# Kernel optimization log

Hardware: AMD Instinct MI355X
Metric: run time of the kernel (lower is better)

Reference implementation:

```python
import jax, jax.numpy as jnp
import numpy as np

B, IN, H = 8192, 1024, 1024

def _ln(x, g, b, eps=1e-5):
    mu = jnp.mean(x, axis=-1, keepdims=True)
    var = jnp.mean(jnp.square(x - mu), axis=-1, keepdims=True)
    return (x - mu) * jax.lax.rsqrt(var + eps) * g + b

def setup_inputs() -> dict:
    key = jax.random.key(0)
    ks = jax.random.split(key, 8)
    s_h = 1.0 / np.sqrt(H)
    s_i = 1.0 / np.sqrt(IN)
    inp = {
        'x': jax.random.normal(ks[0], (B, IN), jnp.float32),
        'h': jax.random.normal(ks[1], (B, H), jnp.float32),
        'W_r': jax.random.uniform(ks[2], (H, H), jnp.float32, -s_h, s_h),
        'U_r': jax.random.uniform(ks[3], (H, IN), jnp.float32, -s_i, s_i),
        'W_u': jax.random.uniform(ks[4], (H, H), jnp.float32, -s_h, s_h),
        'U_u': jax.random.uniform(ks[5], (H, IN), jnp.float32, -s_i, s_i),
        'W_c': jax.random.uniform(ks[6], (H, H), jnp.float32, -s_h, s_h),
        'U_c': jax.random.uniform(ks[7], (H, IN), jnp.float32, -s_i, s_i),
        # LayerNorm params: rows = [r_hidden, r_input, u_hidden, u_input, c_hidden, c_input]
        'ln_gamma': 0.1 * jnp.ones((6, H), jnp.float32),
        'ln_beta': jnp.zeros((6, H), jnp.float32),
    }
    return inp

def reference(x, h, W_r, U_r, W_u, U_u, W_c, U_c, ln_gamma, ln_beta):
    g, b = ln_gamma, ln_beta
    # nn.Linear(bias=False): y = x @ W.T
    r = jax.nn.sigmoid(_ln(h @ W_r.T, g[0], b[0]) + _ln(x @ U_r.T, g[1], b[1]))
    u = jax.nn.sigmoid(_ln(h @ W_u.T, g[2], b[2]) + _ln(x @ U_u.T, g[3], b[3]))
    c = jnp.tanh(_ln((h * r) @ W_c.T, g[4], b[4]) + _ln(x @ U_c.T, g[5], b[5]))
    return (1.0 - u) * h + u * c
```

## Files before the change

kernel.cpp:

```cpp
#include <hip/hip_runtime.h>
#include <cstdint>
#include <cstddef>

typedef unsigned short u16;
typedef unsigned char u8;
typedef __attribute__((ext_vector_type(8))) short bf16x8;
typedef __attribute__((ext_vector_type(4))) float f32x4;
typedef __attribute__((ext_vector_type(4))) int i32x4;
typedef __attribute__((ext_vector_type(8))) int i32x8;

__device__ inline float bf2f(u16 u) { return __uint_as_float(((unsigned)u) << 16); }
__device__ inline unsigned f2bf(float f) {
  unsigned u = __float_as_uint(f);
  u += 0x7fffu + ((u >> 16) & 1u);
  return u >> 16;
}

__device__ inline unsigned f2fp8(float f) {
  unsigned s = (__float_as_uint(f) >> 31) << 7;
  float a = fabsf(f);
  if (a >= 0.015625f) {
    unsigned u = __float_as_uint(a);
    u += 0x7FFFFu + ((u >> 20) & 1u);
    unsigned e = (u >> 23) - 120u;
    unsigned m = (u >> 20) & 7u;
    return s | (e << 3) | m;
  }
  int m = (int)rintf(a * 512.0f);
  return s | (unsigned)m;
}

__device__ inline void async16(const void* g, void* l) {
  __builtin_amdgcn_global_load_lds(
      (const __attribute__((address_space(1))) void*)g,
      (__attribute__((address_space(3))) void*)l, 16, 0, 0);
}

__device__ inline i32x8 join8(i32x4 lo, i32x4 hi) {
  i32x8 r;
  r[0] = lo[0]; r[1] = lo[1]; r[2] = lo[2]; r[3] = lo[3];
  r[4] = hi[0]; r[5] = hi[1]; r[6] = hi[2]; r[7] = hi[3];
  return r;
}

__device__ inline void unpack8(uint4 q, float* o) {
  o[0] = bf2f((u16)(q.x & 0xffffu)); o[1] = bf2f((u16)(q.x >> 16));
  o[2] = bf2f((u16)(q.y & 0xffffu)); o[3] = bf2f((u16)(q.y >> 16));
  o[4] = bf2f((u16)(q.z & 0xffffu)); o[5] = bf2f((u16)(q.z >> 16));
  o[6] = bf2f((u16)(q.w & 0xffffu)); o[7] = bf2f((u16)(q.w >> 16));
}

__device__ inline uint4 pack8(const float* v) {
  uint4 q;
  q.x = f2bf(v[0]) | (f2bf(v[1]) << 16);
  q.y = f2bf(v[2]) | (f2bf(v[3]) << 16);
  q.z = f2bf(v[4]) | (f2bf(v[5]) << 16);
  q.w = f2bf(v[6]) | (f2bf(v[7]) << 16);
  return q;
}

__device__ inline float fast_sigmoid(float z) {
  return 1.0f / (1.0f + exp2f(-1.4426950408889634f * z));
}
__device__ inline float fast_tanh(float z) {
  return 1.0f - 2.0f / (1.0f + exp2f(2.8853900817779268f * z));
}

struct ConvArgs2 {
  const float* x; const float* h; const float* wr; const float* ur;
  const float* wbf[4];
  u16* xb; u16* hb; u8* x8; u8* h8; u8* w8r; u8* w8u;
  u16* wbo[4];
};

__global__ __launch_bounds__(256) void convert_all(ConvArgs2 a) {
  const int b = blockIdx.x;
  const int t = threadIdx.x;
  if (b < 16384) {
    const bool isx = b < 8192;
    const int off = isx ? b : b - 8192;
    const float* __restrict__ s = isx ? a.x : a.h;
    u16* __restrict__ db = isx ? a.xb : a.hb;
    u8*  __restrict__ d8 = isx ? a.x8 : a.h8;
    const int i = (off * 256 + t) * 4;
    float4 v = *(const float4*)(s + i);
    uint2 o;
    o.x = f2bf(v.x) | (f2bf(v.y) << 16);
    o.y = f2bf(v.z) | (f2bf(v.w) << 16);
    *(uint2*)(db + i) = o;
    unsigned q = f2fp8(v.x) | (f2fp8(v.y) << 8) | (f2fp8(v.z) << 16) | (f2fp8(v.w) << 24);
    *(unsigned*)(d8 + i) = q;
  } else if (b < 18432) {
    const bool isr = b < 17408;
    const int off = isr ? b - 16384 : b - 17408;
    const float* __restrict__ s = isr ? a.wr : a.ur;
    u8* __restrict__ d8 = isr ? a.w8r : a.w8u;
    const int i = (off * 256 + t) * 4;
    float4 v = *(const float4*)(s + i);
    unsigned q = f2fp8(v.x * 8192.f) | (f2fp8(v.y * 8192.f) << 8) |
                 (f2fp8(v.z * 8192.f) << 16) | (f2fp8(v.w * 8192.f) << 24);
    *(unsigned*)(d8 + i) = q;
  } else {
    const int tt = b - 18432;
    const int which = tt >> 10;
    const int off = tt & 1023;
    const float* __restrict__ s = a.wbf[which];
    u16* __restrict__ d = a.wbo[which];
    const int i = (off * 256 + t) * 4;
    float4 v = *(const float4*)(s + i);
    uint2 o;
    o.x = f2bf(v.x) | (f2bf(v.y) << 16);
    o.y = f2bf(v.z) | (f2bf(v.w) << 16);
    *(uint2*)(d + i) = o;
  }
}

struct GemmF8 { const u8* A[2]; const u8* Bw[2]; u16* Y[2]; };

__global__ __launch_bounds__(256) void gemm_fp8(GemmF8 args) {
  const int p = blockIdx.x;
  const int xcd = p & 7;
  const int s = p >> 3;
  const int pr = s >> 4;
  const int cc = s & 15;
  const int gate = cc >> 3;
  const int col = cc & 7;
  const int r = pr * 8 + xcd;

  const u8* __restrict__ A  = args.A[gate];
  const u8* __restrict__ Bw = args.Bw[gate];
  u16* __restrict__ Y = args.Y[gate];

  __shared__ __attribute__((aligned(16))) u8 As[128 * 128];
  __shared__ __attribute__((aligned(16))) u8 Bs[128 * 128];

  const int tid  = threadIdx.x;
  const int lane = tid & 63;
  const int w    = tid >> 6;
  const int wm   = w >> 1;
  const int wn   = w & 1;

  const int rowBlk = r * 128;
  const int colBlk = col * 128;

  const int srow = lane >> 3;
  const int scol = ((lane & 7) ^ srow) * 16;
  const u8* gA[4]; const u8* gB[4]; u8* lA[4]; u8* lB[4];
#pragma unroll
  for (int i = 0; i < 4; i++) {
    const int rr = w * 32 + i * 8;
    gA[i] = A  + (size_t)(rowBlk + rr + srow) * 1024 + scol;
    gB[i] = Bw + (size_t)(colBlk + rr + srow) * 1024 + scol;
    lA[i] = &As[rr * 128];
    lB[i] = &Bs[rr * 128];
  }

  const int sw = lane & 7;
  const int g0 = (lane >> 4) * 2;
  const int o0 = ((g0 ^ sw) << 4);
  const int o1 = (((g0 + 1) ^ sw) << 4);
  const int frA = (wm * 64 + (lane & 15)) * 128;
  const int frB = (wn * 64 + (lane & 15)) * 128;

  f32x4 acc[4][4] = {};

  for (int k0 = 0; k0 < 1024; k0 += 128) {
#pragma unroll
    for (int i = 0; i < 4; i++) {
      async16(gA[i] + k0, lA[i]);
      async16(gB[i] + k0, lB[i]);
    }
    __syncthreads();
    i32x8 af[4], bfr[4];
#pragma unroll
    for (int t = 0; t < 4; t++) {
      const int ra = frA + t * 16 * 128;
      const int rb = frB + t * 16 * 128;
      af[t]  = join8(*(const i32x4*)&As[ra + o0], *(const i32x4*)&As[ra + o1]);
      bfr[t] = join8(*(const i32x4*)&Bs[rb + o0], *(const i32x4*)&Bs[rb + o1]);
    }
#pragma unroll
    for (int tm = 0; tm < 4; tm++)
#pragma unroll
      for (int tn = 0; tn < 4; tn++)
        acc[tm][tn] = __builtin_amdgcn_mfma_scale_f32_16x16x128_f8f6f4(
            af[tm], bfr[tn], acc[tm][tn],
            0, 0,
            0, 127,
            0, 114);
    __syncthreads();
  }

  const int rBase = rowBlk + wm * 64 + (lane >> 4) * 4;
  const int cBase = colBlk + wn * 64 + (lane & 15);
#pragma unroll
  for (int tm = 0; tm < 4; tm++) {
#pragma unroll
    for (int i = 0; i < 4; i++) {
      const size_t rr = (size_t)(rBase + tm * 16 + i);
#pragma unroll
      for (int tn = 0; tn < 4; tn++)
        Y[rr * 1024 + cBase + tn * 16] = (u16)f2bf(acc[tm][tn][i]);
    }
  }
}

struct Gemm4 { const u16* A[4]; const u16* Bw[4]; u16* Y[4]; };

__global__ __launch_bounds__(512, 2) void gemm_8ph(Gemm4 args) {
  const int p = blockIdx.x;
  const int wg = (p & 7) * 64 + (p >> 3);
  const int gate = wg >> 7;
  const int rem  = wg & 127;
  const int rblk = rem >> 2;
  const int cblk = rem & 3;

  const u16* __restrict__ A  = args.A[gate];
  const u16* __restrict__ Bw = args.Bw[gate];
  u16* __restrict__ Y = args.Y[gate];

  __shared__ __attribute__((aligned(16))) u16 sm[2][2][2][128 * 64];

  const int tid  = threadIdx.x;
  const int lane = tid & 63;
  const int w    = tid >> 6;
  const int wm   = w >> 2;
  const int wn   = w & 3;

  const int l8   = lane >> 3;
  const int sgrp = (lane & 7) ^ l8;
  const u16* aSrc = A  + ((size_t)(rblk * 256 + w * 8 + l8) << 10) + sgrp * 8;
  const u16* bSrc = Bw + ((size_t)(cblk * 256 + w * 8 + l8) << 10) + sgrp * 8;
  const int ldsW = w * 8 * 64;

  const int fr = (lane & 15) * 64 + ((((lane >> 4) ^ (lane & 7))) << 3);

  f32x4 acc_lo[4][4] = {};
  f32x4 acc_hi[4][4] = {};

  auto stage = [&](const u16* src, int tt, int op, int half) {
    const int d = tt & 1;
    const u16* s = src + (size_t)half * 131072 + tt * 64;
    u16* l0 = &sm[d][op][half][ldsW];
    async16(s, l0);
    async16(s + 65536, l0 + 4096);
  };

  stage(bSrc, 0, 1, 0); stage(bSrc, 0, 1, 1);
  stage(aSrc, 0, 0, 0); stage(aSrc, 0, 0, 1);
  stage(bSrc, 1, 1, 0); stage(bSrc, 1, 1, 1);
  stage(aSrc, 1, 0, 0);
  asm volatile("s_waitcnt vmcnt(6)" ::: "memory");
  __builtin_amdgcn_s_barrier();

  for (int t = 0; t < 16; ++t) {
    const int d = t & 1;
    const u16* baseA = &sm[d][0][wm][0];
    const u16* baseB = &sm[d][1][wn >> 1][(wn & 1) * 4096];

    bf16x8 alo[2][4], bfg[2][4];
#pragma unroll
    for (int kk = 0; kk < 2; ++kk) {
      const int fo = fr ^ (kk << 5);
#pragma unroll
      for (int m = 0; m < 4; ++m) alo[kk][m] = *(const bf16x8*)(baseA + m * 1024 + fo);
#pragma unroll
      for (int n = 0; n < 4; ++n) bfg[kk][n] = *(const bf16x8*)(baseB + n * 1024 + fo);
    }
    if (t + 1 < 16) stage(aSrc, t + 1, 0, 1);
    __builtin_amdgcn_s_barrier();
    asm volatile("s_waitcnt lgkmcnt(0)" ::: "memory");
    __builtin_amdgcn_s_setprio(1);
#pragma unroll
    for (int m = 0; m < 4; ++m)
#pragma unroll
      for (int n = 0; n < 2; ++n)
#pragma unroll
        for (int kk = 0; kk < 2; ++kk)
          acc_lo[m][n] = __builtin_amdgcn_mfma_f32_16x16x32_bf16(alo[kk][m], bfg[kk][n], acc_lo[m][n], 0, 0, 0);
    __builtin_amdgcn_s_setprio(0);
    __builtin_amdgcn_s_barrier();

    if (t + 2 < 16) stage(bSrc, t + 2, 1, 0);
    __builtin_amdgcn_s_barrier();
    __builtin_amdgcn_s_setprio(1);
#pragma unroll
    for (int m = 0; m < 4; ++m)
#pragma unroll
      for (int n = 2; n < 4; ++n)
#pragma unroll
        for (int kk = 0; kk < 2; ++kk)
          acc_lo[m][n] = __builtin_amdgcn_mfma_f32_16x16x32_bf16(alo[kk][m], bfg[kk][n], acc_lo[m][n], 0, 0, 0);
    __builtin_amdgcn_s_setprio(0);
    __builtin_amdgcn_s_barrier();

    bf16x8 ahi[2][4];
#pragma unroll
    for (int kk = 0; kk < 2; ++kk) {
      const int fo = fr ^ (kk << 5);
#pragma unroll
      for (int m = 0; m < 4; ++m) ahi[kk][m] = *(const bf16x8*)(baseA + (m + 4) * 1024 + fo);
    }
    if (t + 2 < 16) stage(bSrc, t + 2, 1, 1);
    __builtin_amdgcn_s_barrier();
    asm volatile("s_waitcnt lgkmcnt(0)" ::: "memory");
    __builtin_amdgcn_s_setprio(1);
#pragma unroll
    for (int m = 0; m < 4; ++m)
#pragma unroll
      for (int n = 0; n < 2; ++n)
#pragma unroll
        for (int kk = 0; kk < 2; ++kk)
          acc_hi[m][n] = __builtin_amdgcn_mfma_f32_16x16x32_bf16(ahi[kk][m], bfg[kk][n], acc_hi[m][n], 0, 0, 0);
    __builtin_amdgcn_s_setprio(0);
    __builtin_amdgcn_s_barrier();

    if (t + 2 < 16) stage(aSrc, t + 2, 0, 0);
    __builtin_amdgcn_s_barrier();
    __builtin_amdgcn_s_setprio(1);
#pragma unroll
    for (int m = 0; m < 4; ++m)
#pragma unroll
      for (int n = 2; n < 4; ++n)
#pragma unroll
        for (int kk = 0; kk < 2; ++kk)
          acc_hi[m][n] = __builtin_amdgcn_mfma_f32_16x16x32_bf16(ahi[kk][m], bfg[kk][n], acc_hi[m][n], 0, 0, 0);
    __builtin_amdgcn_s_setprio(0);
    if (t < 14) asm volatile("s_waitcnt vmcnt(6)" ::: "memory");
    else        asm volatile("s_waitcnt vmcnt(0)" ::: "memory");
    __builtin_amdgcn_s_barrier();
  }

  const int rBase = rblk * 256 + wm * 128 + (lane >> 4) * 4;
  const int cBase = cblk * 256 + wn * 64 + (lane & 15);
#pragma unroll
  for (int m = 0; m < 4; ++m) {
#pragma unroll
    for (int i = 0; i < 4; ++i) {
      const size_t r0 = (size_t)(rBase + m * 16 + i) * 1024 + cBase;
#pragma unroll
      for (int n = 0; n < 4; ++n) {
        Y[r0 + n * 16]             = (u16)f2bf(acc_lo[m][n][i]);
        Y[r0 + 64 * 1024 + n * 16] = (u16)f2bf(acc_hi[m][n][i]);
      }
    }
  }
}

__global__ __launch_bounds__(256) void rgate_kernel(
    const u16* __restrict__ Yrh, const u16* __restrict__ Yrx,
    const u16* __restrict__ hb, const float* __restrict__ gamma,
    const float* __restrict__ beta, u16* __restrict__ hrb) {
  const int row  = blockIdx.x * 4 + (threadIdx.x >> 6);
  const int lane = threadIdx.x & 63;
  const size_t rb = (size_t)row * 1024;

  uint4 qa[2], qb[2], qh[2];
  qa[0] = *(const uint4*)(Yrh + rb + lane * 8);
  qa[1] = *(const uint4*)(Yrh + rb + 512 + lane * 8);
  qb[0] = *(const uint4*)(Yrx + rb + lane * 8);
  qb[1] = *(const uint4*)(Yrx + rb + 512 + lane * 8);
  qh[0] = *(const uint4*)(hb  + rb + lane * 8);
  qh[1] = *(const uint4*)(hb  + rb + 512 + lane * 8);

  float s0 = 0.f, s0q = 0.f, s1 = 0.f, s1q = 0.f;
  float tmp[8];
#pragma unroll
  for (int c = 0; c < 2; c++) {
    unpack8(qa[c], tmp);
#pragma unroll
    for (int j = 0; j < 8; j++) { s0 += tmp[j]; s0q += tmp[j] * tmp[j]; }
    unpack8(qb[c], tmp);
#pragma unroll
    for (int j = 0; j < 8; j++) { s1 += tmp[j]; s1q += tmp[j] * tmp[j]; }
  }
#pragma unroll
  for (int off = 1; off < 64; off <<= 1) {
    s0 += __shfl_xor(s0, off, 64);  s0q += __shfl_xor(s0q, off, 64);
    s1 += __shfl_xor(s1, off, 64);  s1q += __shfl_xor(s1q, off, 64);
  }

  const float inv = 1.0f / 1024.0f;
  const float mu0 = s0 * inv, rs0 = rsqrtf(s0q * inv - mu0 * mu0 + 1e-5f);
  const float mu1 = s1 * inv, rs1 = rsqrtf(s1q * inv - mu1 * mu1 + 1e-5f);

#pragma unroll
  for (int c = 0; c < 2; c++) {
    const int cb = c * 512 + lane * 8;
    float va[8], vb[8], vh[8], o[8];
    unpack8(qa[c], va); unpack8(qb[c], vb); unpack8(qh[c], vh);
#pragma unroll
    for (int j = 0; j < 8; j++) {
      const float ln0 = (va[j] - mu0) * rs0 * gamma[cb + j] + beta[cb + j];
      const float ln1 = (vb[j] - mu1) * rs1 * gamma[1024 + cb + j] + beta[1024 + cb + j];
      const float rg = fast_sigmoid(ln0 + ln1);
      o[j] = vh[j] * rg;
    }
    *(uint4*)(hrb + rb + cb) = pack8(o);
  }
}

__global__ __launch_bounds__(256) void final_fuse(
    const u16* __restrict__ Yuh, const u16* __restrict__ Yux,
    const u16* __restrict__ Ych, const u16* __restrict__ Ycx,
    const float* __restrict__ h, const float* __restrict__ gamma,
    const float* __restrict__ beta, float* __restrict__ out) {
  const int row  = blockIdx.x * 4 + (threadIdx.x >> 6);
  const int lane = threadIdx.x & 63;
  const size_t rb = (size_t)row * 1024;

  uint4 q0[2], q1[2], q2[2], q3[2];
  float4 hf[4];
#pragma unroll
  for (int c = 0; c < 2; c++) {
    const int cb = c * 512 + lane * 8;
    q0[c] = *(const uint4*)(Yuh + rb + cb);
    q1[c] = *(const uint4*)(Yux + rb + cb);
    q2[c] = *(const uint4*)(Ych + rb + cb);
    q3[c] = *(const uint4*)(Ycx + rb + cb);
    hf[c * 2]     = *(const float4*)(h + rb + cb);
    hf[c * 2 + 1] = *(const float4*)(h + rb + cb + 4);
  }

  float s[8] = {0.f, 0.f, 0.f, 0.f, 0.f, 0.f, 0.f, 0.f};
  float tmp[8];
#pragma unroll
  for (int c = 0; c < 2; c++) {
    unpack8(q0[c], tmp);
#pragma unroll
    for (int j = 0; j < 8; j++) { s[0] += tmp[j]; s[1] += tmp[j] * tmp[j]; }
    unpack8(q1[c], tmp);
#pragma unroll
    for (int j = 0; j < 8; j++) { s[2] += tmp[j]; s[3] += tmp[j] * tmp[j]; }
    unpack8(q2[c], tmp);
#pragma unroll
    for (int j = 0; j < 8; j++) { s[4] += tmp[j]; s[5] += tmp[j] * tmp[j]; }
    unpack8(q3[c], tmp);
#pragma unroll
    for (int j = 0; j < 8; j++) { s[6] += tmp[j]; s[7] += tmp[j] * tmp[j]; }
  }
#pragma unroll
  for (int off = 1; off < 64; off <<= 1) {
#pragma unroll
    for (int q = 0; q < 8; q++) s[q] += __shfl_xor(s[q], off, 64);
  }

  const float inv = 1.0f / 1024.0f;
  const float mu0 = s[0] * inv, rs0 = rsqrtf(s[1] * inv - mu0 * mu0 + 1e-5f);
  const float mu1 = s[2] * inv, rs1 = rsqrtf(s[3] * inv - mu1 * mu1 + 1e-5f);
  const float mu2 = s[4] * inv, rs2 = rsqrtf(s[5] * inv - mu2 * mu2 + 1e-5f);
  const float mu3 = s[6] * inv, rs3 = rsqrtf(s[7] * inv - mu3 * mu3 + 1e-5f);

#pragma unroll
  for (int c = 0; c < 2; c++) {
    const int cb = c * 512 + lane * 8;
    float v0[8], v1[8], v2[8], v3[8];
    unpack8(q0[c], v0); unpack8(q1[c], v1); unpack8(q2[c], v2); unpack8(q3[c], v3);
    const float* hv = (const float*)&hf[c * 2];
    float o[8];
#pragma unroll
    for (int j = 0; j < 8; j++) {
      const int cc = cb + j;
      const float ln2 = (v0[j] - mu0) * rs0 * gamma[2 * 1024 + cc] + beta[2 * 1024 + cc];
      const float ln3 = (v1[j] - mu1) * rs1 * gamma[3 * 1024 + cc] + beta[3 * 1024 + cc];
      const float ln4 = (v2[j] - mu2) * rs2 * gamma[4 * 1024 + cc] + beta[4 * 1024 + cc];
      const float ln5 = (v3[j] - mu3) * rs3 * gamma[5 * 1024 + cc] + beta[5 * 1024 + cc];
      const float u  = fast_sigmoid(ln2 + ln3);
      const float cg = fast_tanh(ln4 + ln5);
      o[j] = (1.0f - u) * hv[j] + u * cg;
    }
    *(float4*)(out + rb + cb)     = *(float4*)&o[0];
    *(float4*)(out + rb + cb + 4) = *(float4*)&o[4];
  }
}

extern "C" void kernel_launch(void* const* d_in, const int* in_sizes, int n_in,
                              void* d_out, int out_size, void* d_ws, size_t ws_size,
                              hipStream_t stream) {
  const float* x  = (const float*)d_in[0];
  const float* h  = (const float*)d_in[1];
  const float* W_r = (const float*)d_in[2];
  const float* U_r = (const float*)d_in[3];
  const float* W_u = (const float*)d_in[4];
  const float* U_u = (const float*)d_in[5];
  const float* W_c = (const float*)d_in[6];
  const float* U_c = (const float*)d_in[7];
  const float* gamma = (const float*)d_in[8];
  const float* beta  = (const float*)d_in[9];
  float* out = (float*)d_out;

  char* ws = (char*)d_ws;
  const size_t MB = 1024 * 1024;
  const size_t SZ_ACT = 16 * MB;

  u16* xb = (u16*)(ws);
  u16* hb = (u16*)(ws + 16 * MB);
  u16* wb[4];
  for (int i = 0; i < 4; i++) wb[i] = (u16*)(ws + (32 + 2 * i) * MB);
  u8* w8r = (u8*)(ws + 40 * MB);
  u8* w8u = (u8*)(ws + 41 * MB);
  char* ybase = ws + 42 * MB;
  u16* Y0 = (u16*)(ybase);
  u16* Y1 = (u16*)(ybase + SZ_ACT);
  u16* Y2 = (u16*)(ybase + 2 * SZ_ACT);
  u16* Y3 = (u16*)(ybase + 3 * SZ_ACT);
  u16* Y5 = (u16*)(ybase + 4 * SZ_ACT);
  u8* x8 = (u8*)Y5;
  u8* h8 = (u8*)Y5 + 8 * MB;

  ConvArgs2 ca = {};
  ca.x = x; ca.h = h; ca.wr = W_r; ca.ur = U_r;
  ca.wbf[0] = W_u; ca.wbf[1] = U_u; ca.wbf[2] = W_c; ca.wbf[3] = U_c;
  ca.xb = xb; ca.hb = hb; ca.x8 = x8; ca.h8 = h8; ca.w8r = w8r; ca.w8u = w8u;
  ca.wbo[0] = (u16*)(ws + 32 * MB); ca.wbo[1] = (u16*)(ws + 34 * MB);
  ca.wbo[2] = (u16*)(ws + 36 * MB); ca.wbo[3] = (u16*)(ws + 38 * MB);
  convert_all<<<22528, 256, 0, stream>>>(ca);

  GemmF8 gf = {};
  gf.A[0] = h8; gf.Bw[0] = w8r; gf.Y[0] = Y0;
  gf.A[1] = x8; gf.Bw[1] = w8u; gf.Y[1] = Y1;
  gemm_fp8<<<1024, 256, 0, stream>>>(gf);

  rgate_kernel<<<2048, 256, 0, stream>>>(Y0, Y1, hb, gamma, beta, Y1);

  Gemm4 gb = {};
  gb.A[0] = xb; gb.Bw[0] = wb[1]; gb.Y[0] = Y3;
  gb.A[1] = xb; gb.Bw[1] = wb[3]; gb.Y[1] = Y5;
  gb.A[2] = hb; gb.Bw[2] = wb[0]; gb.Y[2] = Y2;
  gb.A[3] = Y1; gb.Bw[3] = wb[2]; gb.Y[3] = Y0;
  gemm_8ph<<<512, 512, 0, stream>>>(gb);

  final_fuse<<<2048, 256, 0, stream>>>(Y2, Y3, Y0, Y5, h, gamma, beta, out);
}
```

Before: 270.9 us.

## Rewrite FP8 GEMM as 256x256 tiles with double-buffered phased pipeline

Replaces the 128x128, 4-wave FP8 GEMM with a 256x256, 8-wave kernel that double-buffers LDS tiles and interleaves async global->LDS loads with MFMA phases, guarded by explicit barriers, waitcnts and setprio. Larger tiles raise data reuse per block, and the phased schedule is meant to hide load latency that the old load-sync-compute loop exposed. In exchange there are fewer blocks (256 for 256 CUs), higher register and LDS use (128KB LDS per block), and the hand-written vmcnt counts have to stay correct.

After: 270.4 us. About the same (-0.2%).

```diff
diff --git a/kernel.cpp b/kernel.cpp
--- a/kernel.cpp
+++ b/kernel.cpp
@@ -117,90 +117,143 @@
 
 struct GemmF8 { const u8* A[2]; const u8* Bw[2]; u16* Y[2]; };
 
-__global__ __launch_bounds__(256) void gemm_fp8(GemmF8 args) {
+__global__ __launch_bounds__(512, 2) void gemm_fp8(GemmF8 args) {
   const int p = blockIdx.x;
-  const int xcd = p & 7;
-  const int s = p >> 3;
-  const int pr = s >> 4;
-  const int cc = s & 15;
-  const int gate = cc >> 3;
-  const int col = cc & 7;
-  const int r = pr * 8 + xcd;
+  const int wg = (p & 7) * 32 + (p >> 3);
+  const int gate = wg >> 7;
+  const int rem  = wg & 127;
+  const int rblk = rem >> 2;
+  const int cblk = rem & 3;
 
   const u8* __restrict__ A  = args.A[gate];
   const u8* __restrict__ Bw = args.Bw[gate];
   u16* __restrict__ Y = args.Y[gate];
 
-  __shared__ __attribute__((aligned(16))) u8 As[128 * 128];
-  __shared__ __attribute__((aligned(16))) u8 Bs[128 * 128];
+  __shared__ __attribute__((aligned(16))) u8 sm[2][2][2][128 * 128];
 
   const int tid  = threadIdx.x;
   const int lane = tid & 63;
   const int w    = tid >> 6;
-  const int wm   = w >> 1;
-  const int wn   = w & 1;
-
-  const int rowBlk = r * 128;
-  const int colBlk = col * 128;
-
-  const int srow = lane >> 3;
-  const int scol = ((lane & 7) ^ srow) * 16;
-  const u8* gA[4]; const u8* gB[4]; u8* lA[4]; u8* lB[4];
-#pragma unroll
-  for (int i = 0; i < 4; i++) {
-    const int rr = w * 32 + i * 8;
-    gA[i] = A  + (size_t)(rowBlk + rr + srow) * 1024 + scol;
-    gB[i] = Bw + (size_t)(colBlk + rr + srow) * 1024 + scol;
-    lA[i] = &As[rr * 128];
-    lB[i] = &Bs[rr * 128];
-  }
+  const int wm   = w >> 2;
+  const int wn   = w & 3;
+
+  const int l8   = lane >> 3;
+  const int sgrp = (lane & 7) ^ l8;
+  const u8* aSrc = A  + ((size_t)(rblk * 256 + w * 8 + l8) << 10) + sgrp * 16;
+  const u8* bSrc = Bw + ((size_t)(cblk * 256 + w * 8 + l8) << 10) + sgrp * 16;
+  const int ldsW = w * 8 * 128;
 
   const int sw = lane & 7;
   const int g0 = (lane >> 4) * 2;
   const int o0 = ((g0 ^ sw) << 4);
   const int o1 = (((g0 + 1) ^ sw) << 4);
-  const int frA = (wm * 64 + (lane & 15)) * 128;
-  const int frB = (wn * 64 + (lane & 15)) * 128;
-
-  f32x4 acc[4][4] = {};
-
-  for (int k0 = 0; k0 < 1024; k0 += 128) {
-#pragma unroll
-    for (int i = 0; i < 4; i++) {
-      async16(gA[i] + k0, lA[i]);
-      async16(gB[i] + k0, lB[i]);
-    }
-    __syncthreads();
-    i32x8 af[4], bfr[4];
-#pragma unroll
-    for (int t = 0; t < 4; t++) {
-      const int ra = frA + t * 16 * 128;
-      const int rb = frB + t * 16 * 128;
-      af[t]  = join8(*(const i32x4*)&As[ra + o0], *(const i32x4*)&As[ra + o1]);
-      bfr[t] = join8(*(const i32x4*)&Bs[rb + o0], *(const i32x4*)&Bs[rb + o1]);
-    }
-#pragma unroll
-    for (int tm = 0; tm < 4; tm++)
-#pragma unroll
-      for (int tn = 0; tn < 4; tn++)
-        acc[tm][tn] = __builtin_amdgcn_mfma_scale_f32_16x16x128_f8f6f4(
-            af[tm], bfr[tn], acc[tm][tn],
-            0, 0,
-            0, 127,
-            0, 114);
-    __syncthreads();
-  }
-
-  const int rBase = rowBlk + wm * 64 + (lane >> 4) * 4;
-  const int cBase = colBlk + wn * 64 + (lane & 15);
-#pragma unroll
-  for (int tm = 0; tm < 4; tm++) {
-#pragma unroll
-    for (int i = 0; i < 4; i++) {
-      const size_t rr = (size_t)(rBase + tm * 16 + i);
-#pragma unroll
-      for (int tn = 0; tn < 4; tn++)
-        Y[rr * 1024 + cBase + tn * 16] = (u16)f2bf(acc[tm][tn][i]);
+  const int frR = (lane & 15) * 128;
+
+  f32x4 acc_lo[4][4] = {};
+  f32x4 acc_hi[4][4] = {};
+
+  auto stage = [&](const u8* src, int tt, int op, int half) {
+    const int d = tt & 1;
+    const u8* s = src + (size_t)half * 131072 + tt * 128;
+    u8* l0 = &sm[d][op][half][ldsW];
+    async16(s, l0);
+    async16(s + 65536, l0 + 8192);
+  };
+
+  stage(bSrc, 0, 1, 0); stage(bSrc, 0, 1, 1);
+  stage(aSrc, 0, 0, 0); stage(aSrc, 0, 0, 1);
+  stage(bSrc, 1, 1, 0); stage(bSrc, 1, 1, 1);
+  stage(aSrc, 1, 0, 0);
+  asm volatile("s_waitcnt vmcnt(6)" ::: "memory");
+  __builtin_amdgcn_s_barrier();
+
+  for (int t = 0; t < 8; ++t) {
+    const int d = t & 1;
+    const u8* baseA = &sm[d][0][wm][0];
+    const u8* baseB = &sm[d][1][wn >> 1][(wn & 1) * 8192];
+
+    i32x8 alo[4], bfg[4];
+#pragma unroll
+    for (int m = 0; m < 4; ++m) {
+      const int ra = frR + m * 2048;
+      alo[m] = join8(*(const i32x4*)&baseA[ra + o0], *(const i32x4*)&baseA[ra + o1]);
+    }
+#pragma unroll
+    for (int n = 0; n < 4; ++n) {
+      const int rbb = frR + n * 2048;
+      bfg[n] = join8(*(const i32x4*)&baseB[rbb + o0], *(const i32x4*)&baseB[rbb + o1]);
+    }
+    if (t + 1 < 8) stage(aSrc, t + 1, 0, 1);
+    __builtin_amdgcn_s_barrier();
+    asm volatile("s_waitcnt lgkmcnt(0)" ::: "memory");
+    __builtin_amdgcn_s_setprio(1);
+#pragma unroll
+    for (int m = 0; m < 4; ++m)
+#pragma unroll
+      for (int n = 0; n < 2; ++n)
+        acc_lo[m][n] = __builtin_amdgcn_mfma_scale_f32_16x16x128_f8f6f4(
+            alo[m], bfg[n], acc_lo[m][n], 0, 0, 0, 127, 0, 114);
+    __builtin_amdgcn_s_setprio(0);
+    __builtin_amdgcn_s_barrier();
+
+    if (t + 2 < 8) stage(bSrc, t + 2, 1, 0);
+    __builtin_amdgcn_s_barrier();
+    __builtin_amdgcn_s_setprio(1);
+#pragma unroll
+    for (int m = 0; m < 4; ++m)
+#pragma unroll
+      for (int n = 2; n < 4; ++n)
+        acc_lo[m][n] = __builtin_amdgcn_mfma_scale_f32_16x16x128_f8f6f4(
+            alo[m], bfg[n], acc_lo[m][n], 0, 0, 0, 127, 0, 114);
+    __builtin_amdgcn_s_setprio(0);
+    __builtin_amdgcn_s_barrier();
+
+    i32x8 ahi[4];
+#pragma unroll
+    for (int m = 0; m < 4; ++m) {
+      const int ra = frR + m * 2048 + 8192;
+      ahi[m] = join8(*(const i32x4*)&baseA[ra + o0], *(const i32x4*)&baseA[ra + o1]);
+    }
+    if (t + 2 < 8) stage(bSrc, t + 2, 1, 1);
+    __builtin_amdgcn_s_barrier();
+    asm volatile("s_waitcnt lgkmcnt(0)" ::: "memory");
+    __builtin_amdgcn_s_setprio(1);
+#pragma unroll
+    for (int m = 0; m < 4; ++m)
+#pragma unroll
+      for (int n = 0; n < 2; ++n)
+        acc_hi[m][n] = __builtin_amdgcn_mfma_scale_f32_16x16x128_f8f6f4(
+            ahi[m], bfg[n], acc_hi[m][n], 0, 0, 0, 127, 0, 114);
+    __builtin_amdgcn_s_setprio(0);
+    __builtin_amdgcn_s_barrier();
+
+    if (t + 2 < 8) stage(aSrc, t + 2, 0, 0);
+    __builtin_amdgcn_s_barrier();
+    __builtin_amdgcn_s_setprio(1);
+#pragma unroll
+    for (int m = 0; m < 4; ++m)
+#pragma unroll
+      for (int n = 2; n < 4; ++n)
+        acc_hi[m][n] = __builtin_amdgcn_mfma_scale_f32_16x16x128_f8f6f4(
+            ahi[m], bfg[n], acc_hi[m][n], 0, 0, 0, 127, 0, 114);
+    __builtin_amdgcn_s_setprio(0);
+    if (t < 6) asm volatile("s_waitcnt vmcnt(6)" ::: "memory");
+    else       asm volatile("s_waitcnt vmcnt(0)" ::: "memory");
+    __builtin_amdgcn_s_barrier();
+  }
+
+  const int rBase = rblk * 256 + wm * 128 + (lane >> 4) * 4;
+  const int cBase = cblk * 256 + wn * 64 + (lane & 15);
+#pragma unroll
+  for (int m = 0; m < 4; ++m) {
+#pragma unroll
+    for (int i = 0; i < 4; ++i) {
+      const size_t r0 = (size_t)(rBase + m * 16 + i) * 1024 + cBase;
+#pragma unroll
+      for (int n = 0; n < 4; ++n) {
+        Y[r0 + n * 16]             = (u16)f2bf(acc_lo[m][n][i]);
+        Y[r0 + 64 * 1024 + n * 16] = (u16)f2bf(acc_hi[m][n][i]);
+      }
     }
   }
 }
@@ -519,7 +572,7 @@
   GemmF8 gf = {};
   gf.A[0] = h8; gf.Bw[0] = w8r; gf.Y[0] = Y0;
   gf.A[1] = x8; gf.Bw[1] = w8u; gf.Y[1] = Y1;
-  gemm_fp8<<<1024, 256, 0, stream>>>(gf);
+  gemm_fp8<<<256, 512, 0, stream>>>(gf);
 
   rgate_kernel<<<2048, 256, 0, stream>>>(Y0, Y1, hb, gamma, beta, Y1);
 
```
